# Optimization experiments

Measured on AMD Instinct MI355X. Metric: run time of the kernel, lower is better.

The kernel has to match this reference:

```python
import jax, jax.numpy as jnp
from jax import lax
import numpy as np

B, F, K = 2048, 4096, 64  # batch, features (output_size), channels (input_size)
ETA = 1.0  # Dirichlet hyperparameter eta


def setup_inputs() -> dict:
    key = jax.random.key(0)
    k1, k2, k3 = jax.random.split(key, 3)
    x = jax.random.randint(k1, (B, F), 0, 50).astype(jnp.int32)        # observed counts
    theta = jax.random.uniform(k2, (B, K), jnp.float32)                # latent rates (positive)
    phi = jax.random.uniform(k3, (K, F), jnp.float32)                  # unnormalized signatures
    return {"x": x, "theta": theta, "phi": phi}


def _augment_reduce(key, theta, phi, x):
    """Exact multinomial thinning chi_{ijk} ~ Mult(x_ij, theta_ik*phi_kj / sum_k)
    via K sequential conditional binomials; returns the scatter-reduced
    sufficient statistics m_ik = sum_j chi and x_jk = sum_i chi without ever
    materializing the (B, F, K) tensor."""
    Kc = theta.shape[1]
    n0 = x.astype(jnp.float32)                 # (B,F) remaining counts
    denom = theta @ phi                        # (B,F) total unnormalized prob mass
    keys = jax.random.split(key, Kc)

    def step(carry, inp):
        n_rem, den = carry
        kk, th_k, ph_k = inp                   # th_k: (B,), ph_k: (F,)
        p = th_k[:, None] * ph_k[None, :]      # (B,F) mass of channel k
        ratio = jnp.clip(p / jnp.maximum(den, 1e-30), 0.0, 1.0)
        chi = jax.random.binomial(kk, n_rem, ratio, dtype=jnp.float32)  # (B,F)
        return (n_rem - chi, den - p), (chi.sum(axis=1), chi.sum(axis=0))

    _, (m_cols, x_cols) = lax.scan(step, (n0, denom), (keys, theta.T, phi))
    m_ik = m_cols.T                            # (B,K)
    x_jk = x_cols.T                            # (F,K)
    return m_ik, x_jk


def reference(x, theta, phi):
    # phi rows live on the simplex (Dirichlet-distributed in the model)
    phi = phi / phi.sum(axis=-1, keepdims=True)
    key = jax.random.key(42)
    k_aug, k_dir = jax.random.split(key)
    m_ik, x_jk = _augment_reduce(k_aug, theta, phi, x)
    # phi ~ Dir(x_.jk + eta), row-wise over channels: alpha shape (K, F)
    alpha = x_jk.T + ETA
    phi_new = jax.random.dirichlet(k_dir, alpha, dtype=jnp.float32)
    return m_ik, phi_new
```

## Files before the change

kernel.cpp:

```cpp
#include <hip/hip_runtime.h>
#include <stdint.h>

#define BB 2048
#define FF 4096
#define KK 64

#define INV_DEPTH 50
#define BTRS_DEPTH 16

__host__ __device__ __forceinline__ uint32_t rotl32(uint32_t v, int n) {
  return (v << n) | (v >> (32 - n));
}

__host__ __device__ __forceinline__ void tf2x32(uint32_t key0, uint32_t key1,
                                                uint32_t c0, uint32_t c1,
                                                uint32_t& o0, uint32_t& o1) {
  uint32_t ks2 = key0 ^ key1 ^ 0x1BD11BDAu;
  uint32_t x0 = c0 + key0, x1 = c1 + key1;
#define TFR(r) { x0 += x1; x1 = rotl32(x1, (r)); x1 ^= x0; }
  TFR(13) TFR(15) TFR(26) TFR(6)
  x0 += key1; x1 += ks2 + 1u;
  TFR(17) TFR(29) TFR(16) TFR(24)
  x0 += ks2; x1 += key0 + 2u;
  TFR(13) TFR(15) TFR(26) TFR(6)
  x0 += key0; x1 += key1 + 3u;
  TFR(17) TFR(29) TFR(16) TFR(24)
  x0 += key1; x1 += ks2 + 4u;
  TFR(13) TFR(15) TFR(26) TFR(6)
  x0 += ks2; x1 += key0 + 5u;
#undef TFR
  o0 = x0; o1 = x1;
}

__host__ __device__ __forceinline__ void key_child(uint32_t k0, uint32_t k1, uint32_t idx,
                                                   uint32_t& o0, uint32_t& o1) {
  tf2x32(k0, k1, 0u, idx, o0, o1);
}

__device__ __forceinline__ uint32_t rbits(uint32_t k0, uint32_t k1, uint32_t e) {
  uint32_t a, b;
  tf2x32(k0, k1, 0u, e, a, b);
  return a ^ b;
}

__device__ __forceinline__ float u01_from_bits(uint32_t bits) {
  uint32_t fb = (bits >> 9) | 0x3f800000u;
  return __fsub_rn(__uint_as_float(fb), 1.0f);
}

__device__ __forceinline__ float erfinv_f32(float x) {
  float w = -log1pf(-__fmul_rn(x, x));
  float p;
  if (w < 5.0f) {
    w = __fsub_rn(w, 2.5f);
    p = 2.81022636e-08f;
    p = __fadd_rn(3.43273939e-07f, __fmul_rn(p, w));
    p = __fadd_rn(-3.5233877e-06f, __fmul_rn(p, w));
    p = __fadd_rn(-4.39150654e-06f, __fmul_rn(p, w));
    p = __fadd_rn(0.00021858087f, __fmul_rn(p, w));
    p = __fadd_rn(-0.00125372503f, __fmul_rn(p, w));
    p = __fadd_rn(-0.00417768164f, __fmul_rn(p, w));
    p = __fadd_rn(0.246640727f, __fmul_rn(p, w));
    p = __fadd_rn(1.50140941f, __fmul_rn(p, w));
  } else {
    w = __fsub_rn(sqrtf(w), 3.0f);
    p = -0.000200214257f;
    p = __fadd_rn(0.000100950558f, __fmul_rn(p, w));
    p = __fadd_rn(0.00134934322f, __fmul_rn(p, w));
    p = __fadd_rn(-0.00367342844f, __fmul_rn(p, w));
    p = __fadd_rn(0.00573950773f, __fmul_rn(p, w));
    p = __fadd_rn(-0.0076224613f, __fmul_rn(p, w));
    p = __fadd_rn(0.00943887047f, __fmul_rn(p, w));
    p = __fadd_rn(1.00167406f, __fmul_rn(p, w));
    p = __fadd_rn(2.83297682f, __fmul_rn(p, w));
  }
  return __fmul_rn(p, x);
}

__device__ __forceinline__ float normal_from_key(uint32_t k0, uint32_t k1) {
  float u01 = u01_from_bits(rbits(k0, k1, 0u));
  const float lo = -0.99999994f;
  float u = __fadd_rn(__fmul_rn(u01, 2.0f), lo);
  u = fmaxf(lo, u);
  return __fmul_rn(1.41421356f, erfinv_f32(u));
}

__device__ __forceinline__ float stirling_tail(float k) {
  const float tab[10] = {
    0.0810614667953272f, 0.0413406959554092f, 0.0276779256849983f,
    0.02079067210376509f, 0.0166446911898211f, 0.0138761288230707f,
    0.0118967099458917f, 0.0104112652619720f, 0.00925546218271273f,
    0.00833056343336287f};
  if (k <= 9.0f) return tab[(int)k];
  float kp1 = __fadd_rn(k, 1.0f);
  float kp1sq = __fmul_rn(kp1, kp1);
  float inner = __fsub_rn(0.0027777778f, 0.00079365081f / kp1sq);
  float t = __fsub_rn(0.083333336f, inner / kp1sq);
  return t / kp1;
}


__global__ void rowsum_kernel(const float* __restrict__ phi, float* __restrict__ rs) {
  __shared__ float red[256];
  int k = blockIdx.x;
  float s = 0.0f;
  for (int j = threadIdx.x; j < FF; j += 256) s += phi[k * FF + j];
  red[threadIdx.x] = s;
  __syncthreads();
  for (int off = 128; off > 0; off >>= 1) {
    if (threadIdx.x < off) red[threadIdx.x] += red[threadIdx.x + off];
    __syncthreads();
  }
  if (threadIdx.x == 0) rs[k] = red[0];
}

__global__ void chains_kernel(uint32_t ka0, uint32_t ka1, uint32_t* __restrict__ ch) {
  int k = threadIdx.x;
  if (k >= KK) return;
  uint32_t s0, s1;
  key_child(ka0, ka1, (uint32_t)k, s0, s1);

  uint2* inv = (uint2*)ch + k * INV_DEPTH;
  uint2* b0p = (uint2*)(ch + KK * INV_DEPTH * 2) + k * BTRS_DEPTH;
  uint2* b1p = (uint2*)(ch + KK * INV_DEPTH * 2 + KK * BTRS_DEPTH * 2) + k * BTRS_DEPTH;
  uint2* cont = (uint2*)(ch + KK * INV_DEPTH * 2 + KK * BTRS_DEPTH * 4) + k;

  uint32_t c0 = s0, c1 = s1;
  for (int t = 0; t < INV_DEPTH; ++t) {
    uint32_t a, b, n0, n1;
    key_child(c0, c1, 0u, a, b);
    key_child(c0, c1, 1u, n0, n1);
    inv[t] = make_uint2(a, b);
    c0 = n0; c1 = n1;
  }
  c0 = s0; c1 = s1;
  for (int t = 0; t < BTRS_DEPTH; ++t) {
    uint32_t n0, n1, a0, a1, u0, u1;
    key_child(c0, c1, 0u, n0, n1);
    key_child(c0, c1, 1u, a0, a1);
    key_child(c0, c1, 2u, u0, u1);
    b0p[t] = make_uint2(a0, a1);
    b1p[t] = make_uint2(u0, u1);
    c0 = n0; c1 = n1;
  }
  cont[0] = make_uint2(c0, c1);
}

__global__ __launch_bounds__(256) void sample_kernel(
    const int* __restrict__ xin, const float* __restrict__ theta,
    const float* __restrict__ phi, const float* __restrict__ rs,
    float* __restrict__ m_out, float* __restrict__ x_out,
    const uint32_t* __restrict__ ch) {
  __shared__ float phs[KK][64];
  __shared__ float xs[KK][64];
  __shared__ float denl[32][64];
  __shared__ float ml[32][64];
  __shared__ int ctr;

  const uint2* inv_all = (const uint2*)ch;
  const uint2* b0_all = (const uint2*)(ch + KK * INV_DEPTH * 2);
  const uint2* b1_all = (const uint2*)(ch + KK * INV_DEPTH * 2 + KK * BTRS_DEPTH * 2);
  const uint2* cont_all = (const uint2*)(ch + KK * INV_DEPTH * 2 + KK * BTRS_DEPTH * 4);

  int tid = threadIdx.x;
  int jt = blockIdx.x;
  int rg = blockIdx.y;
  int row0 = rg * 32;

  for (int idx = tid; idx < KK * 64; idx += 256) {
    int k = idx >> 6, jl = idx & 63;
    phs[k][jl] = phi[k * FF + jt * 64 + jl] / rs[k];
    xs[k][jl] = 0.0f;
    ml[idx >> 6][jl] = 0.0f;
  }
  for (int idx = tid; idx < 32 * 64; idx += 256) ml[idx >> 6][idx & 63] = 0.0f;
  if (tid == 0) ctr = 0;
  __syncthreads();

  for (int s = tid; s < 32 * 64; s += 256) {
    int il = s >> 6, jl = s & 63;
    const float* tr = theta + (size_t)(row0 + il) * KK;
    float d = 0.0f;
    #pragma unroll 8
    for (int kk = 0; kk < KK; ++kk) d = fmaf(tr[kk], phs[kk][jl], d);
    denl[il][jl] = d;
  }
  __syncthreads();

  int mode = 3;
  int il = 0, jje = 0, k = 0, ti = 0;
  uint32_t e = 0;
  bool plth = true;
  float n = 0, den = 0, p = 0, q = 0, l1p = 0, gs = 0, ng = 0;
  float sB = 0, sA = 0, sC = 0, sVr = 0, sR = 0, sAlf = 0, sMm = 0;

  for (int iter = 0; iter < 300000 && __any(mode != 4); ++iter) {
    if (mode == 3) {
      int tt = atomicAdd(&ctr, 1);
      if (tt >= 32 * 64) {
        mode = 4;
      } else {
        il = tt >> 6; jje = tt & 63;
        int gi = row0 + il, gj = jt * 64 + jje;
        n = (float)xin[gi * FF + gj];
        den = denl[il][jje];
        e = (uint32_t)(gi * FF + gj);
        k = 0;
        mode = 2;
      }
    }
    if (mode == 2) {
      float th = theta[(row0 + il) * KK + k];
      p = __fmul_rn(th, phs[k][jje]);
      float ratio = p / fmaxf(den, 1e-30f);
      ratio = fminf(fmaxf(ratio, 0.0f), 1.0f);
      plth = ratio < 0.5f;
      q = plth ? ratio : __fsub_rn(1.0f, ratio);
      if (n <= 0.0f || q <= 0.0f) {
        float chi = plth ? 0.0f : n;
        if (chi != 0.0f) {
          atomicAdd(&ml[il][k], chi);
          atomicAdd(&xs[k][jje], chi);
        }
        mode = 3;
      } else if (__fmul_rn(n, q) <= 10.0f) {
        l1p = log1pf(-q);
        gs = 0.0f; ng = 0.0f; ti = 0;
        mode = 0;
      } else {
        float stddev = sqrtf(__fmul_rn(__fmul_rn(n, q), __fsub_rn(1.0f, q)));
        sB = __fadd_rn(1.15f, __fmul_rn(2.53f, stddev));
        sA = __fadd_rn(__fadd_rn(-0.0873f, __fmul_rn(0.0248f, sB)), __fmul_rn(0.01f, q));
        sC = __fadd_rn(__fmul_rn(n, q), 0.5f);
        sVr = __fsub_rn(0.92f, 4.2f / sB);
        sR = q / __fsub_rn(1.0f, q);
        sAlf = __fmul_rn(__fadd_rn(2.83f, 5.1f / sB), stddev);
        sMm = floorf(__fmul_rn(__fadd_rn(n, 1.0f), q));
        ti = 0;
        mode = 1;
      }
    }
    if (mode == 0) {
      uint2 sk = inv_all[k * INV_DEPTH + ti];
      ng = __fadd_rn(ng, 1.0f);
      float u = u01_from_bits(rbits(sk.x, sk.y, e));
      float g = ceilf(logf(u) / l1p);
      gs = __fadd_rn(gs, g);
      ti++;
      if (!(gs <= n)) {
        float samp = __fsub_rn(ng, 1.0f);
        float chi = plth ? samp : __fsub_rn(n, samp);
        if (chi != 0.0f) {
          atomicAdd(&ml[il][k], chi);
          atomicAdd(&xs[k][jje], chi);
        }
        n = __fsub_rn(n, chi);
        den = __fsub_rn(den, p);
        k++;
        mode = (n <= 0.0f || k >= KK) ? 3 : 2;
      }
    }
    if (mode == 1) {
      uint32_t s00, s01, s10, s11;
      if (ti < BTRS_DEPTH) {
        uint2 A = b0_all[k * BTRS_DEPTH + ti];
        uint2 Bv = b1_all[k * BTRS_DEPTH + ti];
        s00 = A.x; s01 = A.y; s10 = Bv.x; s11 = Bv.y;
      } else {
        uint2 cc = cont_all[k];
        uint32_t c0 = cc.x, c1 = cc.y;
        for (int tw = BTRS_DEPTH; tw < ti; ++tw) {
          uint32_t a, b; key_child(c0, c1, 0u, a, b); c0 = a; c1 = b;
        }
        key_child(c0, c1, 1u, s00, s01);
        key_child(c0, c1, 2u, s10, s11);
      }
      float u = u01_from_bits(rbits(s00, s01, e));
      float v = u01_from_bits(rbits(s10, s11, e));
      u = __fsub_rn(u, 0.5f);
      float us = __fsub_rn(0.5f, fabsf(u));
      bool accept1 = (us >= 0.07f) && (v <= sVr);
      float kf = floorf(__fadd_rn(__fmul_rn(__fadd_rn(__fmul_rn(2.0f, sA) / us, sB), u), sC));
      bool reject = (kf < 0.0f) || (kf > n);
      float v2 = logf(__fmul_rn(v, sAlf) / __fadd_rn(sA / __fmul_rn(us, us), sB));
      float ub =
        __fadd_rn(
          __fadd_rn(
            __fadd_rn(
              __fmul_rn(__fadd_rn(sMm, 0.5f), logf(__fadd_rn(sMm, 1.0f) / __fmul_rn(sR, __fadd_rn(__fsub_rn(n, sMm), 1.0f)))),
              __fmul_rn(__fadd_rn(n, 1.0f), logf(__fadd_rn(__fsub_rn(n, sMm), 1.0f) / __fadd_rn(__fsub_rn(n, kf), 1.0f)))),
            __fmul_rn(__fadd_rn(kf, 0.5f), logf(__fmul_rn(sR, __fadd_rn(__fsub_rn(n, kf), 1.0f)) / __fadd_rn(kf, 1.0f)))),
          __fsub_rn(__fsub_rn(__fadd_rn(stirling_tail(sMm), stirling_tail(__fsub_rn(n, sMm))),
                              stirling_tail(kf)),
                    stirling_tail(__fsub_rn(n, kf))));
      bool accept2 = v2 <= ub;
      ti++;
      bool done = accept1 || ((!reject) && accept2);
      float samp = done ? kf : -1.0f;
      if (done || ti >= 64) {
        float chi = plth ? samp : __fsub_rn(n, samp);
        if (chi != 0.0f) {
          atomicAdd(&ml[il][k], chi);
          atomicAdd(&xs[k][jje], chi);
        }
        n = __fsub_rn(n, chi);
        den = __fsub_rn(den, p);
        k++;
        mode = (n <= 0.0f || k >= KK) ? 3 : 2;
      }
    }
  }

  __syncthreads();
  for (int idx = tid; idx < 32 * 64; idx += 256) {
    int il2 = idx >> 6, k2 = idx & 63;
    float v = ml[il2][k2];
    if (v != 0.0f) atomicAdd(&m_out[(row0 + il2) * KK + k2], v);
  }
  for (int idx = tid; idx < KK * 64; idx += 256) {
    int k2 = idx >> 6, jl = idx & 63;
    float v = xs[k2][jl];
    if (v != 0.0f) atomicAdd(&x_out[k2 * FF + jt * 64 + jl], v);
  }
}

__global__ void gamma_kernel(float* __restrict__ xphi, uint32_t kd0, uint32_t kd1) {
  int e = blockIdx.x * blockDim.x + threadIdx.x;
  if (e >= KK * FF) return;
  float alpha = __fadd_rn(xphi[e], 1.0f);

  uint32_t k0, k1;
  key_child(kd0, kd1, (uint32_t)e, k0, k1);

  uint32_t nk0, nk1;
  key_child(k0, k1, 0u, nk0, nk1);
  k0 = nk0; k1 = nk1;

  float d = __fsub_rn(alpha, 0.33333334f);
  float cc = 0.33333334f / sqrtf(__fmul_rn(9.0f, d));

  float X = 0.0f, V = 1.0f, U = 2.0f;
  for (int t = 0; t < 256; ++t) {
    bool c1 = U >= __fsub_rn(1.0f, __fmul_rn(0.0331f, __fmul_rn(X, X)));
    bool c2 = logf(U) >= __fadd_rn(__fmul_rn(X, 0.5f),
                                   __fmul_rn(d, __fadd_rn(__fsub_rn(1.0f, V), logf(V))));
    if (!(c1 && c2)) break;
    uint32_t b0, b1, xk0, xk1, Uk0, Uk1;
    key_child(k0, k1, 0u, b0, b1);
    key_child(k0, k1, 1u, xk0, xk1);
    key_child(k0, k1, 2u, Uk0, Uk1);
    k0 = b0; k1 = b1;
    float x = 0.0f, v = -1.0f;
    uint32_t ik0 = xk0, ik1 = xk1;
    for (int s = 0; s < 16 && v <= 0.0f; ++s) {
      uint32_t n2a, n2b, sb0, sb1;
      key_child(ik0, ik1, 0u, n2a, n2b);
      key_child(ik0, ik1, 1u, sb0, sb1);
      ik0 = n2a; ik1 = n2b;
      x = normal_from_key(sb0, sb1);
      v = __fadd_rn(1.0f, __fmul_rn(x, cc));
    }
    X = __fmul_rn(x, x);
    V = __fmul_rn(__fmul_rn(v, v), v);
    U = u01_from_bits(rbits(Uk0, Uk1, 0u));
  }
  xphi[e] = __fadd_rn(logf(d), logf(V));
}

__global__ void rownorm_kernel(float* __restrict__ lg) {
  __shared__ float red[256];
  int k = blockIdx.x;
  float* p = lg + (size_t)k * FF;
  float mx = -INFINITY;
  for (int j = threadIdx.x; j < FF; j += 256) mx = fmaxf(mx, p[j]);
  red[threadIdx.x] = mx;
  __syncthreads();
  for (int off = 128; off > 0; off >>= 1) {
    if (threadIdx.x < off) red[threadIdx.x] = fmaxf(red[threadIdx.x], red[threadIdx.x + off]);
    __syncthreads();
  }
  mx = red[0];
  __syncthreads();
  float s = 0.0f;
  for (int j = threadIdx.x; j < FF; j += 256) s += expf(__fsub_rn(p[j], mx));
  red[threadIdx.x] = s;
  __syncthreads();
  for (int off = 128; off > 0; off >>= 1) {
    if (threadIdx.x < off) red[threadIdx.x] += red[threadIdx.x + off];
    __syncthreads();
  }
  float lse = __fadd_rn(logf(red[0]), mx);
  __syncthreads();
  for (int j = threadIdx.x; j < FF; j += 256) p[j] = expf(__fsub_rn(p[j], lse));
}

extern "C" void kernel_launch(void* const* d_in, const int* in_sizes, int n_in,
                              void* d_out, int out_size, void* d_ws, size_t ws_size,
                              hipStream_t stream) {
  (void)in_sizes; (void)n_in; (void)ws_size;
  const int* xin = (const int*)d_in[0];
  const float* theta = (const float*)d_in[1];
  const float* phi = (const float*)d_in[2];
  float* out = (float*)d_out;
  float* m_out = out;
  float* xphi = out + (size_t)BB * KK;
  float* rs = (float*)d_ws;
  uint32_t* chains = (uint32_t*)d_ws + 64;

  uint32_t ka0, ka1, kd0, kd1;
  tf2x32(0u, 42u, 0u, 0u, ka0, ka1);
  tf2x32(0u, 42u, 0u, 1u, kd0, kd1);

  hipMemsetAsync(d_out, 0, (size_t)out_size * sizeof(float), stream);
  hipLaunchKernelGGL(rowsum_kernel, dim3(KK), dim3(256), 0, stream, phi, rs);
  hipLaunchKernelGGL(chains_kernel, dim3(1), dim3(64), 0, stream, ka0, ka1, chains);
  hipLaunchKernelGGL(sample_kernel, dim3(64, 64), dim3(256), 0, stream,
                     xin, theta, phi, rs, m_out, xphi, chains);
  hipLaunchKernelGGL(gamma_kernel, dim3((KK * FF) / 256), dim3(256), 0, stream, xphi, kd0, kd1);
  hipLaunchKernelGGL(rownorm_kernel, dim3(KK), dim3(256), 0, stream, xphi);
}
```

Before: 5.402 ms.

## Defer BTRS binomial cases to a parked second pass to cut divergence

When a lane hits the large-mean BTRS rejection branch during the main scan, its state (row, column, channel, remaining count, denominator) is packed into a shared-memory park queue and the lane moves on to new work. After the first pass drains, a second work-stealing loop processes only the parked cases, so BTRS lanes run alongside other BTRS lanes instead of mixing with inversion-sampling lanes. This is meant to reduce wavefront divergence between the two sampler modes. It adds shared memory for the queue and duplicates the sampler code, and packing n into 6 bits assumes counts stay below 64.

```diff
diff --git a/kernel.cpp b/kernel.cpp
--- a/kernel.cpp
+++ b/kernel.cpp
@@ -7,6 +7,7 @@
 
 #define INV_DEPTH 50
 #define BTRS_DEPTH 16
+#define PARK_CAP 384
 
 __host__ __device__ __forceinline__ uint32_t rotl32(uint32_t v, int n) {
   return (v << n) | (v >> (32 - n));
@@ -155,7 +156,8 @@
   __shared__ float xs[KK][64];
   __shared__ float denl[32][64];
   __shared__ float ml[32][64];
-  __shared__ int ctr;
+  __shared__ uint2 park[PARK_CAP];
+  __shared__ int ctr, pk_n, pk_claim;
 
   const uint2* inv_all = (const uint2*)ch;
   const uint2* b0_all = (const uint2*)(ch + KK * INV_DEPTH * 2);
@@ -171,10 +173,9 @@
     int k = idx >> 6, jl = idx & 63;
     phs[k][jl] = phi[k * FF + jt * 64 + jl] / rs[k];
     xs[k][jl] = 0.0f;
-    ml[idx >> 6][jl] = 0.0f;
   }
   for (int idx = tid; idx < 32 * 64; idx += 256) ml[idx >> 6][idx & 63] = 0.0f;
-  if (tid == 0) ctr = 0;
+  if (tid == 0) { ctr = 0; pk_n = 0; pk_claim = 0; }
   __syncthreads();
 
   for (int s = tid; s < 32 * 64; s += 256) {
@@ -187,13 +188,14 @@
   }
   __syncthreads();
 
-  int mode = 3;
+  int mode;
   int il = 0, jje = 0, k = 0, ti = 0;
   uint32_t e = 0;
   bool plth = true;
   float n = 0, den = 0, p = 0, q = 0, l1p = 0, gs = 0, ng = 0;
   float sB = 0, sA = 0, sC = 0, sVr = 0, sR = 0, sAlf = 0, sMm = 0;
 
+  mode = 3;
   for (int iter = 0; iter < 300000 && __any(mode != 4); ++iter) {
     if (mode == 3) {
       int tt = atomicAdd(&ctr, 1);
@@ -228,16 +230,24 @@
         gs = 0.0f; ng = 0.0f; ti = 0;
         mode = 0;
       } else {
-        float stddev = sqrtf(__fmul_rn(__fmul_rn(n, q), __fsub_rn(1.0f, q)));
-        sB = __fadd_rn(1.15f, __fmul_rn(2.53f, stddev));
-        sA = __fadd_rn(__fadd_rn(-0.0873f, __fmul_rn(0.0248f, sB)), __fmul_rn(0.01f, q));
-        sC = __fadd_rn(__fmul_rn(n, q), 0.5f);
-        sVr = __fsub_rn(0.92f, 4.2f / sB);
-        sR = q / __fsub_rn(1.0f, q);
-        sAlf = __fmul_rn(__fadd_rn(2.83f, 5.1f / sB), stddev);
-        sMm = floorf(__fmul_rn(__fadd_rn(n, 1.0f), q));
-        ti = 0;
-        mode = 1;
+        int slot = atomicAdd(&pk_n, 1);
+        if (slot < PARK_CAP) {
+          park[slot] = make_uint2((uint32_t)il | ((uint32_t)jje << 5) |
+                                  ((uint32_t)k << 11) | ((uint32_t)(int)n << 17),
+                                  __float_as_uint(den));
+          mode = 3;
+        } else {
+          float stddev = sqrtf(__fmul_rn(__fmul_rn(n, q), __fsub_rn(1.0f, q)));
+          sB = __fadd_rn(1.15f, __fmul_rn(2.53f, stddev));
+          sA = __fadd_rn(__fadd_rn(-0.0873f, __fmul_rn(0.0248f, sB)), __fmul_rn(0.01f, q));
+          sC = __fadd_rn(__fmul_rn(n, q), 0.5f);
+          sVr = __fsub_rn(0.92f, 4.2f / sB);
+          sR = q / __fsub_rn(1.0f, q);
+          sAlf = __fmul_rn(__fadd_rn(2.83f, 5.1f / sB), stddev);
+          sMm = floorf(__fmul_rn(__fadd_rn(n, 1.0f), q));
+          ti = 0;
+          mode = 1;
+        }
       }
     }
     if (mode == 0) {
@@ -295,9 +305,131 @@
                     stirling_tail(__fsub_rn(n, kf))));
       bool accept2 = v2 <= ub;
       ti++;
-      bool done = accept1 || ((!reject) && accept2);
-      float samp = done ? kf : -1.0f;
-      if (done || ti >= 64) {
+      bool done2 = accept1 || ((!reject) && accept2);
+      float samp = done2 ? kf : -1.0f;
+      if (done2 || ti >= 64) {
+        float chi = plth ? samp : __fsub_rn(n, samp);
+        if (chi != 0.0f) {
+          atomicAdd(&ml[il][k], chi);
+          atomicAdd(&xs[k][jje], chi);
+        }
+        n = __fsub_rn(n, chi);
+        den = __fsub_rn(den, p);
+        k++;
+        mode = (n <= 0.0f || k >= KK) ? 3 : 2;
+      }
+    }
+  }
+
+  __syncthreads();
+
+  int pk_total = min(pk_n, PARK_CAP);
+  mode = 3;
+  for (int iter = 0; iter < 300000 && __any(mode != 4); ++iter) {
+    if (mode == 3) {
+      int tt = atomicAdd(&pk_claim, 1);
+      if (tt >= pk_total) {
+        mode = 4;
+      } else {
+        uint2 st = park[tt];
+        il = (int)(st.x & 31u);
+        jje = (int)((st.x >> 5) & 63u);
+        k = (int)((st.x >> 11) & 63u);
+        n = (float)(int)((st.x >> 17) & 63u);
+        den = __uint_as_float(st.y);
+        e = (uint32_t)((row0 + il) * FF + (jt * 64 + jje));
+        mode = 2;
+      }
+    }
+    if (mode == 2) {
+      float th = theta[(row0 + il) * KK + k];
+      p = __fmul_rn(th, phs[k][jje]);
+      float ratio = p / fmaxf(den, 1e-30f);
+      ratio = fminf(fmaxf(ratio, 0.0f), 1.0f);
+      plth = ratio < 0.5f;
+      q = plth ? ratio : __fsub_rn(1.0f, ratio);
+      if (n <= 0.0f || q <= 0.0f) {
+        float chi = plth ? 0.0f : n;
+        if (chi != 0.0f) {
+          atomicAdd(&ml[il][k], chi);
+          atomicAdd(&xs[k][jje], chi);
+        }
+        mode = 3;
+      } else if (__fmul_rn(n, q) <= 10.0f) {
+        l1p = log1pf(-q);
+        gs = 0.0f; ng = 0.0f; ti = 0;
+        mode = 0;
+      } else {
+        float stddev = sqrtf(__fmul_rn(__fmul_rn(n, q), __fsub_rn(1.0f, q)));
+        sB = __fadd_rn(1.15f, __fmul_rn(2.53f, stddev));
+        sA = __fadd_rn(__fadd_rn(-0.0873f, __fmul_rn(0.0248f, sB)), __fmul_rn(0.01f, q));
+        sC = __fadd_rn(__fmul_rn(n, q), 0.5f);
+        sVr = __fsub_rn(0.92f, 4.2f / sB);
+        sR = q / __fsub_rn(1.0f, q);
+        sAlf = __fmul_rn(__fadd_rn(2.83f, 5.1f / sB), stddev);
+        sMm = floorf(__fmul_rn(__fadd_rn(n, 1.0f), q));
+        ti = 0;
+        mode = 1;
+      }
+    }
+    if (mode == 0) {
+      uint2 sk = inv_all[k * INV_DEPTH + ti];
+      ng = __fadd_rn(ng, 1.0f);
+      float u = u01_from_bits(rbits(sk.x, sk.y, e));
+      float g = ceilf(logf(u) / l1p);
+      gs = __fadd_rn(gs, g);
+      ti++;
+      if (!(gs <= n)) {
+        float samp = __fsub_rn(ng, 1.0f);
+        float chi = plth ? samp : __fsub_rn(n, samp);
+        if (chi != 0.0f) {
+          atomicAdd(&ml[il][k], chi);
+          atomicAdd(&xs[k][jje], chi);
+        }
+        n = __fsub_rn(n, chi);
+        den = __fsub_rn(den, p);
+        k++;
+        mode = (n <= 0.0f || k >= KK) ? 3 : 2;
+      }
+    }
+    if (mode == 1) {
+      uint32_t s00, s01, s10, s11;
+      if (ti < BTRS_DEPTH) {
+        uint2 A = b0_all[k * BTRS_DEPTH + ti];
+        uint2 Bv = b1_all[k * BTRS_DEPTH + ti];
+        s00 = A.x; s01 = A.y; s10 = Bv.x; s11 = Bv.y;
+      } else {
+        uint2 cc = cont_all[k];
+        uint32_t c0 = cc.x, c1 = cc.y;
+        for (int tw = BTRS_DEPTH; tw < ti; ++tw) {
+          uint32_t a, b; key_child(c0, c1, 0u, a, b); c0 = a; c1 = b;
+        }
+        key_child(c0, c1, 1u, s00, s01);
+        key_child(c0, c1, 2u, s10, s11);
+      }
+      float u = u01_from_bits(rbits(s00, s01, e));
+      float v = u01_from_bits(rbits(s10, s11, e));
+      u = __fsub_rn(u, 0.5f);
+      float us = __fsub_rn(0.5f, fabsf(u));
+      bool accept1 = (us >= 0.07f) && (v <= sVr);
+      float kf = floorf(__fadd_rn(__fmul_rn(__fadd_rn(__fmul_rn(2.0f, sA) / us, sB), u), sC));
+      bool reject = (kf < 0.0f) || (kf > n);
+      float v2 = logf(__fmul_rn(v, sAlf) / __fadd_rn(sA / __fmul_rn(us, us), sB));
+      float ub =
+        __fadd_rn(
+          __fadd_rn(
+            __fadd_rn(
+              __fmul_rn(__fadd_rn(sMm, 0.5f), logf(__fadd_rn(sMm, 1.0f) / __fmul_rn(sR, __fadd_rn(__fsub_rn(n, sMm), 1.0f)))),
+              __fmul_rn(__fadd_rn(n, 1.0f), logf(__fadd_rn(__fsub_rn(n, sMm), 1.0f) / __fadd_rn(__fsub_rn(n, kf), 1.0f)))),
+            __fmul_rn(__fadd_rn(kf, 0.5f), logf(__fmul_rn(sR, __fadd_rn(__fsub_rn(n, kf), 1.0f)) / __fadd_rn(kf, 1.0f)))),
+          __fsub_rn(__fsub_rn(__fadd_rn(stirling_tail(sMm), stirling_tail(__fsub_rn(n, sMm))),
+                              stirling_tail(kf)),
+                    stirling_tail(__fsub_rn(n, kf))));
+      bool accept2 = v2 <= ub;
+      ti++;
+      bool done2 = accept1 || ((!reject) && accept2);
+      float samp = done2 ? kf : -1.0f;
+      if (done2 || ti >= 64) {
         float chi = plth ? samp : __fsub_rn(n, samp);
         if (chi != 0.0f) {
           atomicAdd(&ml[il][k], chi);
```

Result: no change. 5.495 ms (+1.7%).
